# Performance work log

Measured on AMD Instinct MI355X. Metric: run time of the kernel, lower is better.

The kernel has to match this reference:

```python
import jax, jax.numpy as jnp
import numpy as np

B, N, D, DEG = 1, 1024, 64, 64
K = 1.0  # Lorentz curvature parameter


def _ln(x, eps=1e-6):
    mu = jnp.mean(x, -1, keepdims=True)
    var = jnp.var(x, -1, keepdims=True)
    return (x - mu) / jnp.sqrt(var + eps)


def setup_inputs() -> dict:
    key = jax.random.key(0)
    ks = jax.random.split(key, 8)
    # valid Lorentz points: time = sqrt(||space||^2 + K)
    xs = jax.random.normal(ks[0], (B, N, D - 1), dtype=jnp.float32)
    x0 = jnp.sqrt(jnp.sum(xs ** 2, -1, keepdims=True) + K)
    x = jnp.concatenate([x0, xs], -1)
    # deterministic adjacency: node i -> (i+1..i+DEG) mod N, exactly E=N*DEG edges
    rows = np.repeat(np.arange(N), DEG)
    cols = (rows + np.tile(np.arange(1, DEG + 1), N)) % N
    adj_np = np.zeros((B, N, N), dtype=bool)
    adj_np[0, rows, cols] = True
    adj = jnp.asarray(adj_np)
    e = jax.random.normal(ks[1], (B, N, N, D), dtype=jnp.float32) * 0.1
    def lin(k, fo, fi):
        return jax.random.normal(k, (fo, fi), dtype=jnp.float32) / np.sqrt(fi).astype(np.float32)
    return dict(
        x=x, adj=adj, e=e, num_edges=B * N * DEG,
        W_edge=lin(ks[2], D, 3 * D), b_edge=jnp.zeros((D,), jnp.float32),
        W_node=lin(ks[3], D, 2 * D), b_node=jnp.zeros((D,), jnp.float32),
        W_hyp=lin(ks[4], D - 1, D), b_hyp=jnp.zeros((D - 1,), jnp.float32),
        W_ada=lin(ks[5], 2 * D, 1), b_ada=jnp.zeros((2 * D,), jnp.float32),
        W_adan=lin(ks[6], 3 * D, D), b_adan=jnp.zeros((3 * D,), jnp.float32),
    )


def reference(x, adj, e, num_edges, W_edge, b_edge, W_node, b_node, W_hyp, b_hyp, W_ada, b_ada, W_adan, b_adan):
    Bx, Nx, Dx = x.shape
    # manifold.logmap0 at origin o=(sqrt(K),0,..): tangent has time component 0
    x0 = x[..., :1]
    xs = x[..., 1:]
    xn = jnp.maximum(jnp.linalg.norm(xs, axis=-1, keepdims=True), 1e-7)
    u = jnp.sqrt(K) * jnp.arccosh(jnp.maximum(x0 / jnp.sqrt(K), 1.0 + 1e-7)) * xs / xn
    xt = jnp.concatenate([jnp.zeros_like(x0), u], -1)  # [B,N,D]
    # edge list (static size)
    bi, ii, jj = jnp.nonzero(adj, size=num_edges)
    hi = xt[bi, ii]          # [E,D]
    hj = xt[bi, jj]          # [E,D]
    ef = e[bi, ii, jj]       # [E,D]
    # Lorentz distance, per-edge (same math as dense cdist + gather)
    inner = -hi[:, 0] * hj[:, 0] + jnp.sum(hi[:, 1:] * hj[:, 1:], -1)
    dist = jnp.clip(jnp.sqrt(K) * jnp.arccosh(jnp.maximum(-inner / K, 1.0 + 1e-7)), 1e-6, 100.0)
    # adaLN modulation from distance: SiLU -> Linear(1, 2D)
    ada = jax.nn.silu(dist[:, None]) @ W_ada.T + b_ada      # [E,2D]
    shift, scale = jnp.split(ada, 2, axis=1)
    ei = jnp.concatenate([hi, hj, ef], -1) @ W_edge.T + b_edge  # [E,D]
    efu = _ln(ei) * (1.0 + scale) + shift                   # [E,D]
    # node model: scatter-mean by source node index into B*N slots (faithful)
    xf = xt.reshape(Bx * Nx, Dx)
    agg = jax.ops.segment_sum(efu, ii, num_segments=Bx * Nx)
    cnt = jax.ops.segment_sum(jnp.ones_like(dist), ii, num_segments=Bx * Nx)
    agg = agg / jnp.maximum(cnt, 1.0)[:, None]
    adan = jax.nn.silu(agg) @ W_adan.T + b_adan             # [B*N,3D]
    sh, sc, gate = jnp.split(adan, 3, axis=1)
    h = xf + gate * (_ln(jnp.concatenate([xf, agg], -1) @ W_node.T + b_node) * (1.0 + sc) + sh)
    # LorentzHypLinear: project space then recompute time
    sp = h @ W_hyp.T + b_hyp                                # [B*N,D-1]
    t = jnp.sqrt(jnp.sum(sp ** 2, -1, keepdims=True) + K)
    out = jnp.concatenate([t, sp], -1) * jnp.sqrt(K / K)    # manifold_out.k == manifold.k
    return out.reshape(Bx, Nx, Dx)
```

## Files before the change

kernel.cpp:

```cpp
#include <hip/hip_runtime.h>

#define N_NODES 1024
#define D 64
#define FSTRIDE 200

typedef __bf16 bf16x8 __attribute__((ext_vector_type(8)));
typedef float f32x4 __attribute__((ext_vector_type(4)));

__device__ __forceinline__ float wave_reduce_sum(float v) {
#pragma unroll
    for (int m = 32; m >= 1; m >>= 1) v += __shfl_xor(v, m, 64);
    return v;
}

__global__ __launch_bounds__(64) void xt_kernel(const float* __restrict__ x,
                                                float* __restrict__ xt) {
    const int i = blockIdx.x;
    const int l = threadIdx.x;
    float v = x[i * D + l];
    float s = (l >= 1) ? v * v : 0.f;
    s = wave_reduce_sum(s);
    float xn = fmaxf(sqrtf(s), 1e-7f);
    float x0 = __shfl(v, 0, 64);
    float z = fmaxf(x0, 1.0f + 1e-7f);
    float ach = logf(z + sqrtf((z - 1.f) * (z + 1.f)));
    float u = (l >= 1) ? ach * v / xn : 0.f;
    xt[i * D + l] = u;
}

__global__ __launch_bounds__(256) void node_kernel(
    const float* __restrict__ xt, const float* __restrict__ eg,
    const float* __restrict__ W_edge, const float* __restrict__ b_edge,
    const float* __restrict__ W_node, const float* __restrict__ b_node,
    const float* __restrict__ W_hyp, const float* __restrict__ b_hyp,
    const float* __restrict__ W_ada, const float* __restrict__ b_ada,
    const float* __restrict__ W_adan, const float* __restrict__ b_adan,
    float* __restrict__ out) {
    __shared__ __align__(16) char smem[52992];
    __bf16* s_F = (__bf16*)smem;
    __bf16* s_G = (__bf16*)(smem + 25600);
    float* s_wada = (float*)(smem + 51200);
    float* s_bada = (float*)(smem + 51712);
    float* s_sd   = (float*)(smem + 52224);
    float* s_hi   = (float*)(smem + 52480);
    float* s_be   = (float*)(smem + 52736);
    float* s_aggw = (float*)smem;
    float* s_agg  = (float*)(smem + 1024);
    float* s_sagg = (float*)(smem + 1280);
    float* s_adan = (float*)(smem + 1536);
    float* s_h    = (float*)(smem + 2304);

    const int i = blockIdx.x;
    const int t = threadIdx.x;
    const int w = t >> 6;
    const int l = t & 63;
    const int m = l & 15;
    const int q = l >> 4;

    if (t < 128) { s_wada[t] = W_ada[t]; s_bada[t] = b_ada[t]; }
    if (t < 64)  { s_hi[t] = xt[i * D + t]; s_be[t] = b_edge[t]; }

#pragma unroll
    for (int r = 0; r < 16; ++r) {
        int n = w * 16 + r;
        const float* wrow = W_edge + n * 192;
        s_G[n * FSTRIDE + l]       = (__bf16)wrow[l];
        s_G[n * FSTRIDE + 64 + l]  = (__bf16)wrow[64 + l];
        s_G[n * FSTRIDE + 128 + l] = (__bf16)wrow[128 + l];
    }

    const float hvf = xt[i * D + l];
    const __bf16 hib = (__bf16)hvf;
    float prod[16];
#pragma unroll
    for (int el = 0; el < 16; ++el) {
        int e = w * 16 + el;
        int j = (i + e + 1) & (N_NODES - 1);
        float hjv = xt[j * D + l];
        float efv = eg[((size_t)i * N_NODES + j) * D + l];
        prod[el] = hvf * hjv;
        s_F[e * FSTRIDE + l]       = hib;
        s_F[e * FSTRIDE + 64 + l]  = (__bf16)hjv;
        s_F[e * FSTRIDE + 128 + l] = (__bf16)efv;
    }
#pragma unroll
    for (int el = 0; el < 16; ++el) {
#pragma unroll
        for (int msk = 32; msk >= 1; msk >>= 1)
            prod[el] += __shfl_xor(prod[el], msk, 64);
    }
#pragma unroll
    for (int el = 0; el < 16; ++el) {
        float zz = fmaxf(-prod[el], 1.0f + 1e-7f);
        float dist = logf(zz + sqrtf((zz - 1.f) * (zz + 1.f)));
        dist = fminf(fmaxf(dist, 1e-6f), 100.f);
        float sdv = dist / (1.f + expf(-dist));
        if (l == el) s_sd[w * 16 + el] = sdv;
    }
    __syncthreads();

    f32x4 acc[4] = {};
    const bf16x8* Arow = (const bf16x8*)(s_F + (w * 16 + m) * FSTRIDE);
#pragma unroll
    for (int ks = 0; ks < 6; ++ks) {
        bf16x8 af = Arow[ks * 4 + q];
#pragma unroll
        for (int nt = 0; nt < 4; ++nt) {
            const bf16x8* Brow = (const bf16x8*)(s_G + (nt * 16 + m) * FSTRIDE);
            bf16x8 bf = Brow[ks * 4 + q];
            acc[nt] = __builtin_amdgcn_mfma_f32_16x16x32_bf16(af, bf, acc[nt], 0, 0, 0);
        }
    }
    __syncthreads();

    float vv[4][4];
    float s1[4] = {0.f, 0.f, 0.f, 0.f}, s2[4] = {0.f, 0.f, 0.f, 0.f};
#pragma unroll
    for (int nt = 0; nt < 4; ++nt) {
        float be = s_be[nt * 16 + m];
#pragma unroll
        for (int r = 0; r < 4; ++r) {
            float x = acc[nt][r] + be;
            vv[nt][r] = x;
            s1[r] += x;
            s2[r] += x * x;
        }
    }
#pragma unroll
    for (int msk = 1; msk <= 8; msk <<= 1) {
#pragma unroll
        for (int r = 0; r < 4; ++r) {
            s1[r] += __shfl_xor(s1[r], msk, 64);
            s2[r] += __shfl_xor(s2[r], msk, 64);
        }
    }
    float colp[4] = {0.f, 0.f, 0.f, 0.f};
#pragma unroll
    for (int r = 0; r < 4; ++r) {
        float mu = s1[r] * (1.f / 64.f);
        float var = s2[r] * (1.f / 64.f) - mu * mu;
        float inv = 1.f / sqrtf(var + 1e-6f);
        float sd = s_sd[w * 16 + q * 4 + r];
#pragma unroll
        for (int nt = 0; nt < 4; ++nt) {
            int n = nt * 16 + m;
            float ln = (vv[nt][r] - mu) * inv;
            float scale = sd * s_wada[64 + n] + s_bada[64 + n];
            float shift = sd * s_wada[n] + s_bada[n];
            colp[nt] += ln * (1.f + scale) + shift;
        }
    }
#pragma unroll
    for (int nt = 0; nt < 4; ++nt) {
        colp[nt] += __shfl_xor(colp[nt], 16, 64);
        colp[nt] += __shfl_xor(colp[nt], 32, 64);
    }
    if (q == 0) {
#pragma unroll
        for (int nt = 0; nt < 4; ++nt) s_aggw[w * 64 + nt * 16 + m] = colp[nt];
    }
    __syncthreads();

    if (t < 64) {
        float agg = (s_aggw[t] + s_aggw[64 + t] + s_aggw[128 + t] + s_aggw[192 + t]) * (1.f / 64.f);
        s_agg[t] = agg;
        s_sagg[t] = agg / (1.f + expf(-agg));
    }
    __syncthreads();

    if (t < 192) {
        float a = b_adan[t];
        const float* wr = &W_adan[t * 64];
#pragma unroll 8
        for (int k = 0; k < 64; ++k) a += wr[k] * s_sagg[k];
        s_adan[t] = a;
    }
    __syncthreads();

    if (w == 0) {
        float nv = b_node[l];
        const float* wr = &W_node[l * 128];
#pragma unroll 8
        for (int k = 0; k < 64; ++k) nv += wr[k] * s_hi[k];
#pragma unroll 8
        for (int k = 0; k < 64; ++k) nv += wr[64 + k] * s_agg[k];
        float r1 = wave_reduce_sum(nv);
        float r2 = wave_reduce_sum(nv * nv);
        float mu = r1 * (1.f / 64.f);
        float var = r2 * (1.f / 64.f) - mu * mu;
        float ln = (nv - mu) / sqrtf(var + 1e-6f);
        float sh = s_adan[l], sc = s_adan[64 + l], gate = s_adan[128 + l];
        float h = s_hi[l] + gate * (ln * (1.f + sc) + sh);
        s_h[l] = h;

        float sp = 0.f;
        if (l >= 1) {
            const float* wr2 = &W_hyp[(l - 1) * 64];
            sp = b_hyp[l - 1];
#pragma unroll 8
            for (int k = 0; k < 64; ++k) sp += wr2[k] * s_h[k];
        }
        float ss = wave_reduce_sum(sp * sp);
        float tt = sqrtf(ss + 1.0f);
        out[i * D + l] = (l == 0) ? tt : sp;
    }
}

extern "C" void kernel_launch(void* const* d_in, const int* in_sizes, int n_in,
                              void* d_out, int out_size, void* d_ws, size_t ws_size,
                              hipStream_t stream) {
    const float* x      = (const float*)d_in[0];
    const float* eg     = (const float*)d_in[2];
    const float* W_edge = (const float*)d_in[4];
    const float* b_edge = (const float*)d_in[5];
    const float* W_node = (const float*)d_in[6];
    const float* b_node = (const float*)d_in[7];
    const float* W_hyp  = (const float*)d_in[8];
    const float* b_hyp  = (const float*)d_in[9];
    const float* W_ada  = (const float*)d_in[10];
    const float* b_ada  = (const float*)d_in[11];
    const float* W_adan = (const float*)d_in[12];
    const float* b_adan = (const float*)d_in[13];
    float* xt  = (float*)d_ws;
    float* out = (float*)d_out;

    xt_kernel<<<N_NODES, 64, 0, stream>>>(x, xt);
    node_kernel<<<N_NODES, 256, 0, stream>>>(xt, eg, W_edge, b_edge, W_node, b_node,
                                             W_hyp, b_hyp, W_ada, b_ada, W_adan, b_adan, out);
}
```

Before: 352.9 us.

## Pre-convert W_edge to bf16 once and read MFMA B operand from global

A new prep kernel converts W_edge to bf16 once per call into workspace. The node kernel then reads MFMA B fragments straight from global/L2 and no longer stages a per-block bf16 copy in LDS. This removes the per-block fp32 load, convert and LDS write, and halves shared memory use, which can raise occupancy. The small GEMVs for W_adan, W_node and W_hyp now use float4 loads. The cost is an extra kernel launch and uncoalesced per-lane global reads for the B operand.

```diff
diff --git a/kernel.cpp b/kernel.cpp
--- a/kernel.cpp
+++ b/kernel.cpp
@@ -5,12 +5,21 @@
 #define FSTRIDE 200
 
 typedef __bf16 bf16x8 __attribute__((ext_vector_type(8)));
+typedef __bf16 bf16x4 __attribute__((ext_vector_type(4)));
 typedef float f32x4 __attribute__((ext_vector_type(4)));
 
 __device__ __forceinline__ float wave_reduce_sum(float v) {
 #pragma unroll
     for (int m = 32; m >= 1; m >>= 1) v += __shfl_xor(v, m, 64);
     return v;
+}
+
+__global__ __launch_bounds__(256) void prep_kernel(const float* __restrict__ W_edge,
+                                                   __bf16* __restrict__ Wb) {
+    int idx = blockIdx.x * 256 + threadIdx.x;
+    float4 v = ((const float4*)W_edge)[idx];
+    bf16x4 o = {(__bf16)v.x, (__bf16)v.y, (__bf16)v.z, (__bf16)v.w};
+    ((bf16x4*)Wb)[idx] = o;
 }
 
 __global__ __launch_bounds__(64) void xt_kernel(const float* __restrict__ x,
@@ -30,20 +39,19 @@
 
 __global__ __launch_bounds__(256) void node_kernel(
     const float* __restrict__ xt, const float* __restrict__ eg,
-    const float* __restrict__ W_edge, const float* __restrict__ b_edge,
+    const __bf16* __restrict__ Wb, const float* __restrict__ b_edge,
     const float* __restrict__ W_node, const float* __restrict__ b_node,
     const float* __restrict__ W_hyp, const float* __restrict__ b_hyp,
     const float* __restrict__ W_ada, const float* __restrict__ b_ada,
     const float* __restrict__ W_adan, const float* __restrict__ b_adan,
     float* __restrict__ out) {
-    __shared__ __align__(16) char smem[52992];
+    __shared__ __align__(16) char smem[27392];
     __bf16* s_F = (__bf16*)smem;
-    __bf16* s_G = (__bf16*)(smem + 25600);
-    float* s_wada = (float*)(smem + 51200);
-    float* s_bada = (float*)(smem + 51712);
-    float* s_sd   = (float*)(smem + 52224);
-    float* s_hi   = (float*)(smem + 52480);
-    float* s_be   = (float*)(smem + 52736);
+    float* s_wada = (float*)(smem + 25600);
+    float* s_bada = (float*)(smem + 26112);
+    float* s_sd   = (float*)(smem + 26624);
+    float* s_hi   = (float*)(smem + 26880);
+    float* s_be   = (float*)(smem + 27136);
     float* s_aggw = (float*)smem;
     float* s_agg  = (float*)(smem + 1024);
     float* s_sagg = (float*)(smem + 1280);
@@ -59,15 +67,6 @@
 
     if (t < 128) { s_wada[t] = W_ada[t]; s_bada[t] = b_ada[t]; }
     if (t < 64)  { s_hi[t] = xt[i * D + t]; s_be[t] = b_edge[t]; }
-
-#pragma unroll
-    for (int r = 0; r < 16; ++r) {
-        int n = w * 16 + r;
-        const float* wrow = W_edge + n * 192;
-        s_G[n * FSTRIDE + l]       = (__bf16)wrow[l];
-        s_G[n * FSTRIDE + 64 + l]  = (__bf16)wrow[64 + l];
-        s_G[n * FSTRIDE + 128 + l] = (__bf16)wrow[128 + l];
-    }
 
     const float hvf = xt[i * D + l];
     const __bf16 hib = (__bf16)hvf;
@@ -101,14 +100,14 @@
 
     f32x4 acc[4] = {};
     const bf16x8* Arow = (const bf16x8*)(s_F + (w * 16 + m) * FSTRIDE);
+    const bf16x8* Wb8 = (const bf16x8*)Wb;
 #pragma unroll
     for (int ks = 0; ks < 6; ++ks) {
         bf16x8 af = Arow[ks * 4 + q];
 #pragma unroll
         for (int nt = 0; nt < 4; ++nt) {
-            const bf16x8* Brow = (const bf16x8*)(s_G + (nt * 16 + m) * FSTRIDE);
-            bf16x8 bf = Brow[ks * 4 + q];
-            acc[nt] = __builtin_amdgcn_mfma_f32_16x16x32_bf16(af, bf, acc[nt], 0, 0, 0);
+            bf16x8 bfr = Wb8[(nt * 16 + m) * 24 + ks * 4 + q];
+            acc[nt] = __builtin_amdgcn_mfma_f32_16x16x32_bf16(af, bfr, acc[nt], 0, 0, 0);
         }
     }
     __syncthreads();
@@ -170,20 +169,33 @@
 
     if (t < 192) {
         float a = b_adan[t];
-        const float* wr = &W_adan[t * 64];
-#pragma unroll 8
-        for (int k = 0; k < 64; ++k) a += wr[k] * s_sagg[k];
+        const float4* wr = (const float4*)(W_adan + t * 64);
+#pragma unroll
+        for (int k = 0; k < 16; ++k) {
+            float4 wv = wr[k];
+            a += wv.x * s_sagg[4 * k] + wv.y * s_sagg[4 * k + 1] +
+                 wv.z * s_sagg[4 * k + 2] + wv.w * s_sagg[4 * k + 3];
+        }
         s_adan[t] = a;
     }
     __syncthreads();
 
     if (w == 0) {
         float nv = b_node[l];
-        const float* wr = &W_node[l * 128];
-#pragma unroll 8
-        for (int k = 0; k < 64; ++k) nv += wr[k] * s_hi[k];
-#pragma unroll 8
-        for (int k = 0; k < 64; ++k) nv += wr[64 + k] * s_agg[k];
+        const float4* wr = (const float4*)(W_node + l * 128);
+#pragma unroll
+        for (int k = 0; k < 16; ++k) {
+            float4 wv = wr[k];
+            nv += wv.x * s_hi[4 * k] + wv.y * s_hi[4 * k + 1] +
+                  wv.z * s_hi[4 * k + 2] + wv.w * s_hi[4 * k + 3];
+        }
+#pragma unroll
+        for (int k = 16; k < 32; ++k) {
+            float4 wv = wr[k];
+            int b = 4 * (k - 16);
+            nv += wv.x * s_agg[b] + wv.y * s_agg[b + 1] +
+                  wv.z * s_agg[b + 2] + wv.w * s_agg[b + 3];
+        }
         float r1 = wave_reduce_sum(nv);
         float r2 = wave_reduce_sum(nv * nv);
         float mu = r1 * (1.f / 64.f);
@@ -195,10 +207,14 @@
 
         float sp = 0.f;
         if (l >= 1) {
-            const float* wr2 = &W_hyp[(l - 1) * 64];
+            const float4* wr2 = (const float4*)(W_hyp + (l - 1) * 64);
             sp = b_hyp[l - 1];
-#pragma unroll 8
-            for (int k = 0; k < 64; ++k) sp += wr2[k] * s_h[k];
+#pragma unroll
+            for (int k = 0; k < 16; ++k) {
+                float4 wv = wr2[k];
+                sp += wv.x * s_h[4 * k] + wv.y * s_h[4 * k + 1] +
+                      wv.z * s_h[4 * k + 2] + wv.w * s_h[4 * k + 3];
+            }
         }
         float ss = wave_reduce_sum(sp * sp);
         float tt = sqrtf(ss + 1.0f);
@@ -221,10 +237,12 @@
     const float* b_ada  = (const float*)d_in[11];
     const float* W_adan = (const float*)d_in[12];
     const float* b_adan = (const float*)d_in[13];
-    float* xt  = (float*)d_ws;
-    float* out = (float*)d_out;
-
+    float*  xt = (float*)d_ws;
+    __bf16* Wb = (__bf16*)((char*)d_ws + 262144);
+
+    prep_kernel<<<12, 256, 0, stream>>>(W_edge, Wb);
     xt_kernel<<<N_NODES, 64, 0, stream>>>(x, xt);
-    node_kernel<<<N_NODES, 256, 0, stream>>>(xt, eg, W_edge, b_edge, W_node, b_node,
-                                             W_hyp, b_hyp, W_ada, b_ada, W_adan, b_adan, out);
-}
+    node_kernel<<<N_NODES, 256, 0, stream>>>(xt, eg, Wb, b_edge, W_node, b_node,
+                                             W_hyp, b_hyp, W_ada, b_ada, W_adan, b_adan,
+                                             (float*)d_out);
+}
```

After: 353.4 us. Within noise of the previous version (+0.1%).
